# Kernel optimization log

Measured on AMD Instinct MI355X. Metric: run time of the kernel, lower is better.

## Reference

```python
import jax, jax.numpy as jnp
import numpy as np

N = 50000      # num nodes
E = 800000     # num edges
C = 512        # channels
ALPHA = 0.1
BETA = float(np.log(0.5 / 1 + 1.0))  # GCN2Conv: beta = log(theta/layer + 1)


def setup_inputs() -> dict:
    key = jax.random.key(0)
    k1, k2, k3, k4, k5 = jax.random.split(key, 5)
    x = jax.random.normal(k1, (N, C), dtype=jnp.float32)
    x0 = jax.random.normal(k2, (N, C), dtype=jnp.float32)
    W1 = jax.random.normal(k3, (C, C), dtype=jnp.float32) * (1.0 / np.sqrt(C))
    edge_weight = jax.random.uniform(k4, (E,), dtype=jnp.float32)
    edge_index = jax.random.randint(k5, (2, E), 0, N, dtype=jnp.int64)
    return {"x": x, "x0": x0, "W1": W1, "edge_weight": edge_weight,
            "edge_index": edge_index}


def reference(x, x0, W1, edge_weight, edge_index):
    src, dst = edge_index[0], edge_index[1]
    # propagate: message = x_j * edge_weight, sum-aggregate at target nodes
    msg = x[src] * edge_weight[:, None]                  # [E, C]
    agg = jax.ops.segment_sum(msg, dst, num_segments=N)  # [N, C]
    # residual blend: x*(1-alpha) + alpha*x_0
    h = agg * (1.0 - ALPHA) + ALPHA * x0                 # [N, C]
    # addmm: (1-beta)*h + beta*(h @ W1)
    out = (1.0 - BETA) * h + BETA * (h @ W1)
    return out
```

## Files before the change

kernel.cpp:

```cpp
#include <hip/hip_runtime.h>
#include <stdint.h>

#define NN 50000
#define NE 800000
#define CH 512

__device__ __forceinline__ unsigned short f2bf(float f) {
    union { float f; unsigned u; } v; v.f = f;
    unsigned u = v.u;
    unsigned r = u + 0x7FFFu + ((u >> 16) & 1u);
    return (unsigned short)(r >> 16);
}

__device__ __forceinline__ float u2f(unsigned u) {
    union { unsigned u; float f; } v; v.u = u;
    return v.f;
}

typedef short bf16x8 __attribute__((ext_vector_type(8)));
typedef float f32x4 __attribute__((ext_vector_type(4)));
typedef float f32x4e __attribute__((ext_vector_type(4)));
typedef unsigned u32x4e __attribute__((ext_vector_type(4)));

__global__ __launch_bounds__(256) void prologue(const f32x4e* __restrict__ x,
                                                u32x4e* __restrict__ xb,
                                                const float* __restrict__ W1,
                                                unsigned short* __restrict__ W1T,
                                                int* __restrict__ cnt) {
    int gid = blockIdx.x * 256 + threadIdx.x;
    {
        f32x4e a = __builtin_nontemporal_load(&x[2 * gid]);
        f32x4e b = __builtin_nontemporal_load(&x[2 * gid + 1]);
        u32x4e o;
        o.x = (unsigned)f2bf(a.x) | ((unsigned)f2bf(a.y) << 16);
        o.y = (unsigned)f2bf(a.z) | ((unsigned)f2bf(a.w) << 16);
        o.z = (unsigned)f2bf(b.x) | ((unsigned)f2bf(b.y) << 16);
        o.w = (unsigned)f2bf(b.z) | ((unsigned)f2bf(b.w) << 16);
        xb[gid] = o;
    }
    if (gid < CH * CH) {
        const float BETA = 0.40546510810816438f;
        const float OMB  = (float)(1.0 - 0.40546510810816438);
        int n = gid >> 9;
        int k = gid & 511;
        float v = BETA * W1[k * 512 + n] + (k == n ? OMB : 0.0f);
        W1T[gid] = f2bf(v);
    }
    if (gid < NN) cnt[gid] = 0;
}

__global__ void hist(const int* __restrict__ ei, int* __restrict__ cnt) {
    int e = blockIdx.x * 256 + threadIdx.x;
    if (e < NE) atomicAdd(&cnt[ei[NE + e]], 1);
}

#define SCAN_B 196

__global__ __launch_bounds__(256) void scan1(const int* __restrict__ cnt, int* __restrict__ bsum) {
    __shared__ int red[4];
    int t = threadIdx.x;
    int i = blockIdx.x * 256 + t;
    int v = (i < NN) ? cnt[i] : 0;
#pragma unroll
    for (int off = 32; off; off >>= 1) v += __shfl_xor(v, off, 64);
    if ((t & 63) == 0) red[t >> 6] = v;
    __syncthreads();
    if (t == 0) bsum[blockIdx.x] = red[0] + red[1] + red[2] + red[3];
}

__global__ __launch_bounds__(256) void scan2(int* __restrict__ bsum, int* __restrict__ boff) {
    __shared__ int ls[256];
    int t = threadIdx.x;
    int v = (t < SCAN_B) ? bsum[t] : 0;
    ls[t] = v;
    __syncthreads();
    for (int off = 1; off < 256; off <<= 1) {
        int add = (t >= off) ? ls[t - off] : 0;
        __syncthreads();
        ls[t] += add;
        __syncthreads();
    }
    if (t < SCAN_B) boff[t] = ls[t] - v;
}

__global__ __launch_bounds__(256) void scan3(const int* __restrict__ cnt, const int* __restrict__ boff,
                                             int* __restrict__ rowptr, int* __restrict__ cursor) {
    __shared__ int ls[256];
    int t = threadIdx.x;
    int i = blockIdx.x * 256 + t;
    int v = (i < NN) ? cnt[i] : 0;
    ls[t] = v;
    __syncthreads();
    for (int off = 1; off < 256; off <<= 1) {
        int add = (t >= off) ? ls[t - off] : 0;
        __syncthreads();
        ls[t] += add;
        __syncthreads();
    }
    if (i < NN) {
        int pre = ls[t] - v + boff[blockIdx.x];
        rowptr[i] = pre;
        cursor[i] = pre;
    }
}

__global__ void fill_slots(const int* __restrict__ ei, const float* __restrict__ ew,
                           int* __restrict__ cursor, int2* __restrict__ eiw) {
    int e = blockIdx.x * 256 + threadIdx.x;
    if (e < NE) {
        int d = ei[NE + e];
        int p = atomicAdd(&cursor[d], 1);
        int2 sw;
        sw.x = ei[e];
        sw.y = __float_as_int(0.9f * ew[e]);
        eiw[p] = sw;
    }
}

__global__ __launch_bounds__(256) void gather_nodes(const u32x4e* __restrict__ xb,
                                                    const f32x4e* __restrict__ x0,
                                                    const int* __restrict__ rowptr,
                                                    const int* __restrict__ cnt,
                                                    const int2* __restrict__ eiw,
                                                    unsigned short* __restrict__ hb) {
    int node = blockIdx.x * 4 + (threadIdx.x >> 6);
    if (node >= NN) return;
    int lane = threadIdx.x & 63;

    const f32x4e* x0r = (const f32x4e*)(x0 + (size_t)node * (CH / 4));
    f32x4e a0 = __builtin_nontemporal_load(&x0r[lane * 2]);
    f32x4e a1 = __builtin_nontemporal_load(&x0r[lane * 2 + 1]);
    float acc[8];
    acc[0] = 0.1f * a0.x; acc[1] = 0.1f * a0.y; acc[2] = 0.1f * a0.z; acc[3] = 0.1f * a0.w;
    acc[4] = 0.1f * a1.x; acc[5] = 0.1f * a1.y; acc[6] = 0.1f * a1.z; acc[7] = 0.1f * a1.w;

    int i = rowptr[node];
    int end = i + cnt[node];

#define ACCUM(vv, ww)                                    \
    acc[0] += (ww) * u2f((vv).x << 16);                  \
    acc[1] += (ww) * u2f((vv).x & 0xffff0000u);          \
    acc[2] += (ww) * u2f((vv).y << 16);                  \
    acc[3] += (ww) * u2f((vv).y & 0xffff0000u);          \
    acc[4] += (ww) * u2f((vv).z << 16);                  \
    acc[5] += (ww) * u2f((vv).z & 0xffff0000u);          \
    acc[6] += (ww) * u2f((vv).w << 16);                  \
    acc[7] += (ww) * u2f((vv).w & 0xffff0000u);

    for (; i + 8 <= end; i += 8) {
        int2 e[8];
#pragma unroll
        for (int j = 0; j < 8; ++j) e[j] = eiw[i + j];
        u32x4e v[8];
#pragma unroll
        for (int j = 0; j < 8; ++j) v[j] = xb[(size_t)e[j].x * (CH / 8) + lane];
#pragma unroll
        for (int j = 0; j < 8; ++j) { float w = __int_as_float(e[j].y); ACCUM(v[j], w) }
    }
    for (; i + 2 <= end; i += 2) {
        int2 e0 = eiw[i], e1 = eiw[i + 1];
        u32x4e v0 = xb[(size_t)e0.x * (CH / 8) + lane];
        u32x4e v1 = xb[(size_t)e1.x * (CH / 8) + lane];
        float w0 = __int_as_float(e0.y), w1 = __int_as_float(e1.y);
        ACCUM(v0, w0)
        ACCUM(v1, w1)
    }
    for (; i < end; ++i) {
        int2 e0 = eiw[i];
        u32x4e v0 = xb[(size_t)e0.x * (CH / 8) + lane];
        float w0 = __int_as_float(e0.y);
        ACCUM(v0, w0)
    }
#undef ACCUM

    u32x4e o;
    o.x = (unsigned)f2bf(acc[0]) | ((unsigned)f2bf(acc[1]) << 16);
    o.y = (unsigned)f2bf(acc[2]) | ((unsigned)f2bf(acc[3]) << 16);
    o.z = (unsigned)f2bf(acc[4]) | ((unsigned)f2bf(acc[5]) << 16);
    o.w = (unsigned)f2bf(acc[6]) | ((unsigned)f2bf(acc[7]) << 16);
    *(u32x4e*)(hb + (size_t)node * CH + lane * 8) = o;
}

__global__ __launch_bounds__(512) void gemm_out(const unsigned short* __restrict__ hb,
                                                const unsigned short* __restrict__ W1T,
                                                float* __restrict__ out) {
    __shared__ unsigned short Al[128 * 64];
    __shared__ unsigned short Bl[256 * 64];
    int t = threadIdx.x;
    int lane = t & 63, w = t >> 6;
    int wm = w & 1, wn = w >> 1;
    int rowBase = blockIdx.y * 128;
    int colBase = blockIdx.x * 256;

    f32x4 acc[4][4] = {};

    for (int k0 = 0; k0 < 512; k0 += 64) {
#pragma unroll
        for (int p = 0; p < 2; ++p) {
            int row = p * 64 + (t >> 3);
            int k8 = (t & 7) * 8;
            uint4 v = *(const uint4*)(hb + (size_t)(rowBase + row) * 512 + k0 + k8);
            int addr = (row * 128 + k8 * 2) ^ ((row & 7) << 4);
            *(uint4*)((char*)Al + addr) = v;
        }
#pragma unroll
        for (int p = 0; p < 4; ++p) {
            int col = p * 64 + (t >> 3);
            int k8 = (t & 7) * 8;
            uint4 v = *(const uint4*)(W1T + (size_t)(colBase + col) * 512 + k0 + k8);
            int addr = (col * 128 + k8 * 2) ^ ((col & 7) << 4);
            *(uint4*)((char*)Bl + addr) = v;
        }
        __syncthreads();

#pragma unroll
        for (int kk = 0; kk < 2; ++kk) {
            bf16x8 af[4], bfr[4];
            int kb = kk * 32 + (lane >> 4) * 8;
#pragma unroll
            for (int mi = 0; mi < 4; ++mi) {
                int row = wm * 64 + mi * 16 + (lane & 15);
                int addr = (row * 128 + kb * 2) ^ ((row & 7) << 4);
                af[mi] = *(const bf16x8*)((const char*)Al + addr);
            }
#pragma unroll
            for (int ni = 0; ni < 4; ++ni) {
                int col = wn * 64 + ni * 16 + (lane & 15);
                int addr = (col * 128 + kb * 2) ^ ((col & 7) << 4);
                bfr[ni] = *(const bf16x8*)((const char*)Bl + addr);
            }
#pragma unroll
            for (int mi = 0; mi < 4; ++mi)
#pragma unroll
                for (int ni = 0; ni < 4; ++ni)
                    acc[mi][ni] = __builtin_amdgcn_mfma_f32_16x16x32_bf16(
                        af[mi], bfr[ni], acc[mi][ni], 0, 0, 0);
        }
        __syncthreads();
    }

#pragma unroll
    for (int mi = 0; mi < 4; ++mi) {
#pragma unroll
        for (int j = 0; j < 4; ++j) {
            int grow = rowBase + wm * 64 + mi * 16 + (lane >> 4) * 4 + j;
            if (grow < NN) {
#pragma unroll
                for (int ni = 0; ni < 4; ++ni) {
                    __builtin_nontemporal_store(
                        acc[mi][ni][j],
                        &out[(size_t)grow * 512 + colBase + wn * 64 + ni * 16 + (lane & 15)]);
                }
            }
        }
    }
}

extern "C" void kernel_launch(void* const* d_in, const int* in_sizes, int n_in,
                              void* d_out, int out_size, void* d_ws, size_t ws_size,
                              hipStream_t stream) {
    const float* x  = (const float*)d_in[0];
    const float* x0 = (const float*)d_in[1];
    const float* W1 = (const float*)d_in[2];
    const float* ew = (const float*)d_in[3];
    const int*   ei = (const int*)d_in[4];
    float* out = (float*)d_out;

    char* ws = (char*)d_ws;
    unsigned short* hb   = (unsigned short*)(ws);
    unsigned short* W1T  = (unsigned short*)(ws + 51249152);
    int*   cnt    = (int*)(ws + 51773440);
    int*   rowptr = (int*)(ws + 51973440);
    int*   cursor = (int*)(ws + 52173440);
    int2*  eiw    = (int2*)(ws + 52373440);
    int*   bsum   = (int*)(ws + 58773440);
    int*   boff   = (int*)(ws + 58774464);

    u32x4e* xb = (u32x4e*)d_out;

    prologue<<<NN * CH / 8 / 256, 256, 0, stream>>>((const f32x4e*)x, xb, W1, W1T, cnt);
    hist<<<(NE + 255) / 256, 256, 0, stream>>>(ei, cnt);
    scan1<<<SCAN_B, 256, 0, stream>>>(cnt, bsum);
    scan2<<<1, 256, 0, stream>>>(bsum, boff);
    scan3<<<SCAN_B, 256, 0, stream>>>(cnt, boff, rowptr, cursor);
    fill_slots<<<(NE + 255) / 256, 256, 0, stream>>>(ei, ew, cursor, eiw);
    gather_nodes<<<(NN + 3) / 4, 256, 0, stream>>>(xb, (const f32x4e*)x0, rowptr, cnt, eiw, hb);
    gemm_out<<<dim3(2, 391), 512, 0, stream>>>(hb, W1T, out);
}
```

Before: 303.2 us.

## Fuse neighbor gather and GEMM into one kernel with LDS-resident rows

Merges the gather/aggregate kernel and the bf16 GEMM into a single kernel. Each 512-thread block aggregates 32 nodes into a swizzled LDS tile, then multiplies that tile by the full W1T, read directly from global memory. This removes the round trip of the intermediate h matrix through HBM and one kernel launch. The bf16 copy of x moves from the output buffer into workspace. The cost is that every block rereads the whole weight matrix without LDS staging, and the GEMM phase waits on the slowest wave's gather.

```diff
diff --git a/kernel.cpp b/kernel.cpp
--- a/kernel.cpp
+++ b/kernel.cpp
@@ -117,25 +117,17 @@
     }
 }
 
-__global__ __launch_bounds__(256) void gather_nodes(const u32x4e* __restrict__ xb,
-                                                    const f32x4e* __restrict__ x0,
-                                                    const int* __restrict__ rowptr,
-                                                    const int* __restrict__ cnt,
-                                                    const int2* __restrict__ eiw,
-                                                    unsigned short* __restrict__ hb) {
-    int node = blockIdx.x * 4 + (threadIdx.x >> 6);
-    if (node >= NN) return;
-    int lane = threadIdx.x & 63;
-
-    const f32x4e* x0r = (const f32x4e*)(x0 + (size_t)node * (CH / 4));
-    f32x4e a0 = __builtin_nontemporal_load(&x0r[lane * 2]);
-    f32x4e a1 = __builtin_nontemporal_load(&x0r[lane * 2 + 1]);
-    float acc[8];
-    acc[0] = 0.1f * a0.x; acc[1] = 0.1f * a0.y; acc[2] = 0.1f * a0.z; acc[3] = 0.1f * a0.w;
-    acc[4] = 0.1f * a1.x; acc[5] = 0.1f * a1.y; acc[6] = 0.1f * a1.z; acc[7] = 0.1f * a1.w;
-
-    int i = rowptr[node];
-    int end = i + cnt[node];
+__global__ __launch_bounds__(512, 4) void fused_gg(const u32x4e* __restrict__ xb,
+                                                   const f32x4e* __restrict__ x0,
+                                                   const int* __restrict__ rowptr,
+                                                   const int* __restrict__ cnt,
+                                                   const int2* __restrict__ eiw,
+                                                   const unsigned short* __restrict__ W1T,
+                                                   float* __restrict__ out) {
+    __shared__ unsigned short Al[32 * 512];
+    int t = threadIdx.x;
+    int lane = t & 63, w = t >> 6;
+    int rowBase = blockIdx.x * 32;
 
 #define ACCUM(vv, ww)                                    \
     acc[0] += (ww) * u2f((vv).x << 16);                  \
@@ -147,109 +139,89 @@
     acc[6] += (ww) * u2f((vv).w << 16);                  \
     acc[7] += (ww) * u2f((vv).w & 0xffff0000u);
 
-    for (; i + 8 <= end; i += 8) {
-        int2 e[8];
-#pragma unroll
-        for (int j = 0; j < 8; ++j) e[j] = eiw[i + j];
-        u32x4e v[8];
-#pragma unroll
-        for (int j = 0; j < 8; ++j) v[j] = xb[(size_t)e[j].x * (CH / 8) + lane];
-#pragma unroll
-        for (int j = 0; j < 8; ++j) { float w = __int_as_float(e[j].y); ACCUM(v[j], w) }
-    }
-    for (; i + 2 <= end; i += 2) {
-        int2 e0 = eiw[i], e1 = eiw[i + 1];
-        u32x4e v0 = xb[(size_t)e0.x * (CH / 8) + lane];
-        u32x4e v1 = xb[(size_t)e1.x * (CH / 8) + lane];
-        float w0 = __int_as_float(e0.y), w1 = __int_as_float(e1.y);
-        ACCUM(v0, w0)
-        ACCUM(v1, w1)
-    }
-    for (; i < end; ++i) {
-        int2 e0 = eiw[i];
-        u32x4e v0 = xb[(size_t)e0.x * (CH / 8) + lane];
-        float w0 = __int_as_float(e0.y);
-        ACCUM(v0, w0)
+    for (int q = 0; q < 4; ++q) {
+        int row = w * 4 + q;
+        int node = rowBase + row;
+        float acc[8] = {0.f, 0.f, 0.f, 0.f, 0.f, 0.f, 0.f, 0.f};
+        if (node < NN) {
+            const f32x4e* x0r = x0 + (size_t)node * (CH / 4);
+            f32x4e a0 = __builtin_nontemporal_load(&x0r[lane * 2]);
+            f32x4e a1 = __builtin_nontemporal_load(&x0r[lane * 2 + 1]);
+            acc[0] = 0.1f * a0.x; acc[1] = 0.1f * a0.y; acc[2] = 0.1f * a0.z; acc[3] = 0.1f * a0.w;
+            acc[4] = 0.1f * a1.x; acc[5] = 0.1f * a1.y; acc[6] = 0.1f * a1.z; acc[7] = 0.1f * a1.w;
+
+            int i   = __builtin_amdgcn_readfirstlane(rowptr[node]);
+            int end = i + __builtin_amdgcn_readfirstlane(cnt[node]);
+            for (; i + 8 <= end; i += 8) {
+                int2 e[8];
+#pragma unroll
+                for (int j = 0; j < 8; ++j) e[j] = eiw[i + j];
+                u32x4e v[8];
+#pragma unroll
+                for (int j = 0; j < 8; ++j) v[j] = xb[(size_t)e[j].x * (CH / 8) + lane];
+#pragma unroll
+                for (int j = 0; j < 8; ++j) { float ww = __int_as_float(e[j].y); ACCUM(v[j], ww) }
+            }
+            for (; i + 2 <= end; i += 2) {
+                int2 e0 = eiw[i], e1 = eiw[i + 1];
+                u32x4e v0 = xb[(size_t)e0.x * (CH / 8) + lane];
+                u32x4e v1 = xb[(size_t)e1.x * (CH / 8) + lane];
+                float w0 = __int_as_float(e0.y), w1 = __int_as_float(e1.y);
+                ACCUM(v0, w0)
+                ACCUM(v1, w1)
+            }
+            for (; i < end; ++i) {
+                int2 e0 = eiw[i];
+                u32x4e v0 = xb[(size_t)e0.x * (CH / 8) + lane];
+                float w0 = __int_as_float(e0.y);
+                ACCUM(v0, w0)
+            }
+        }
+        uint4 o;
+        o.x = (unsigned)f2bf(acc[0]) | ((unsigned)f2bf(acc[1]) << 16);
+        o.y = (unsigned)f2bf(acc[2]) | ((unsigned)f2bf(acc[3]) << 16);
+        o.z = (unsigned)f2bf(acc[4]) | ((unsigned)f2bf(acc[5]) << 16);
+        o.w = (unsigned)f2bf(acc[6]) | ((unsigned)f2bf(acc[7]) << 16);
+        *(uint4*)((char*)Al + row * 1024 + ((lane * 16) ^ ((row & 7) << 4))) = o;
     }
 #undef ACCUM
-
-    u32x4e o;
-    o.x = (unsigned)f2bf(acc[0]) | ((unsigned)f2bf(acc[1]) << 16);
-    o.y = (unsigned)f2bf(acc[2]) | ((unsigned)f2bf(acc[3]) << 16);
-    o.z = (unsigned)f2bf(acc[4]) | ((unsigned)f2bf(acc[5]) << 16);
-    o.w = (unsigned)f2bf(acc[6]) | ((unsigned)f2bf(acc[7]) << 16);
-    *(u32x4e*)(hb + (size_t)node * CH + lane * 8) = o;
-}
-
-__global__ __launch_bounds__(512) void gemm_out(const unsigned short* __restrict__ hb,
-                                                const unsigned short* __restrict__ W1T,
-                                                float* __restrict__ out) {
-    __shared__ unsigned short Al[128 * 64];
-    __shared__ unsigned short Bl[256 * 64];
-    int t = threadIdx.x;
-    int lane = t & 63, w = t >> 6;
-    int wm = w & 1, wn = w >> 1;
-    int rowBase = blockIdx.y * 128;
-    int colBase = blockIdx.x * 256;
-
-    f32x4 acc[4][4] = {};
-
-    for (int k0 = 0; k0 < 512; k0 += 64) {
-#pragma unroll
-        for (int p = 0; p < 2; ++p) {
-            int row = p * 64 + (t >> 3);
-            int k8 = (t & 7) * 8;
-            uint4 v = *(const uint4*)(hb + (size_t)(rowBase + row) * 512 + k0 + k8);
-            int addr = (row * 128 + k8 * 2) ^ ((row & 7) << 4);
-            *(uint4*)((char*)Al + addr) = v;
-        }
-#pragma unroll
-        for (int p = 0; p < 4; ++p) {
-            int col = p * 64 + (t >> 3);
-            int k8 = (t & 7) * 8;
-            uint4 v = *(const uint4*)(W1T + (size_t)(colBase + col) * 512 + k0 + k8);
-            int addr = (col * 128 + k8 * 2) ^ ((col & 7) << 4);
-            *(uint4*)((char*)Bl + addr) = v;
-        }
-        __syncthreads();
-
-#pragma unroll
-        for (int kk = 0; kk < 2; ++kk) {
-            bf16x8 af[4], bfr[4];
-            int kb = kk * 32 + (lane >> 4) * 8;
-#pragma unroll
-            for (int mi = 0; mi < 4; ++mi) {
-                int row = wm * 64 + mi * 16 + (lane & 15);
-                int addr = (row * 128 + kb * 2) ^ ((row & 7) << 4);
-                af[mi] = *(const bf16x8*)((const char*)Al + addr);
-            }
-#pragma unroll
-            for (int ni = 0; ni < 4; ++ni) {
-                int col = wn * 64 + ni * 16 + (lane & 15);
-                int addr = (col * 128 + kb * 2) ^ ((col & 7) << 4);
-                bfr[ni] = *(const bf16x8*)((const char*)Bl + addr);
-            }
-#pragma unroll
-            for (int mi = 0; mi < 4; ++mi)
-#pragma unroll
-                for (int ni = 0; ni < 4; ++ni)
-                    acc[mi][ni] = __builtin_amdgcn_mfma_f32_16x16x32_bf16(
-                        af[mi], bfr[ni], acc[mi][ni], 0, 0, 0);
-        }
-        __syncthreads();
-    }
-
-#pragma unroll
-    for (int mi = 0; mi < 4; ++mi) {
+    __syncthreads();
+
+    f32x4 acc2[2][4] = {};
+    int kg = lane >> 4;
+    int kb = kg * 8;
+    for (int k0 = 0; k0 < 512; k0 += 32) {
+        bf16x8 af[2], bfr[4];
+#pragma unroll
+        for (int mi = 0; mi < 2; ++mi) {
+            int row = mi * 16 + (lane & 15);
+            af[mi] = *(const bf16x8*)((const char*)Al + row * 1024 +
+                                      (((k0 + kb) * 2) ^ ((row & 7) << 4)));
+        }
+#pragma unroll
+        for (int ni = 0; ni < 4; ++ni) {
+            int col = w * 64 + ni * 16 + (lane & 15);
+            bfr[ni] = *(const bf16x8*)(W1T + (size_t)col * 512 + k0 + kb);
+        }
+#pragma unroll
+        for (int mi = 0; mi < 2; ++mi)
+#pragma unroll
+            for (int ni = 0; ni < 4; ++ni)
+                acc2[mi][ni] = __builtin_amdgcn_mfma_f32_16x16x32_bf16(
+                    af[mi], bfr[ni], acc2[mi][ni], 0, 0, 0);
+    }
+
+#pragma unroll
+    for (int mi = 0; mi < 2; ++mi) {
 #pragma unroll
         for (int j = 0; j < 4; ++j) {
-            int grow = rowBase + wm * 64 + mi * 16 + (lane >> 4) * 4 + j;
+            int grow = rowBase + mi * 16 + kg * 4 + j;
             if (grow < NN) {
 #pragma unroll
                 for (int ni = 0; ni < 4; ++ni) {
                     __builtin_nontemporal_store(
-                        acc[mi][ni][j],
-                        &out[(size_t)grow * 512 + colBase + wn * 64 + ni * 16 + (lane & 15)]);
+                        acc2[mi][ni][j],
+                        &out[(size_t)grow * 512 + w * 64 + ni * 16 + (lane & 15)]);
                 }
             }
         }
@@ -267,7 +239,7 @@
     float* out = (float*)d_out;
 
     char* ws = (char*)d_ws;
-    unsigned short* hb   = (unsigned short*)(ws);
+    u32x4e* xb           = (u32x4e*)(ws);
     unsigned short* W1T  = (unsigned short*)(ws + 51249152);
     int*   cnt    = (int*)(ws + 51773440);
     int*   rowptr = (int*)(ws + 51973440);
@@ -276,14 +248,12 @@
     int*   bsum   = (int*)(ws + 58773440);
     int*   boff   = (int*)(ws + 58774464);
 
-    u32x4e* xb = (u32x4e*)d_out;
-
     prologue<<<NN * CH / 8 / 256, 256, 0, stream>>>((const f32x4e*)x, xb, W1, W1T, cnt);
     hist<<<(NE + 255) / 256, 256, 0, stream>>>(ei, cnt);
     scan1<<<SCAN_B, 256, 0, stream>>>(cnt, bsum);
     scan2<<<1, 256, 0, stream>>>(bsum, boff);
     scan3<<<SCAN_B, 256, 0, stream>>>(cnt, boff, rowptr, cursor);
     fill_slots<<<(NE + 255) / 256, 256, 0, stream>>>(ei, ew, cursor, eiw);
-    gather_nodes<<<(NN + 3) / 4, 256, 0, stream>>>(xb, (const f32x4e*)x0, rowptr, cnt, eiw, hb);
-    gemm_out<<<dim3(2, 391), 512, 0, stream>>>(hb, W1T, out);
-}
+    fused_gg<<<(NN + 31) / 32, 512, 0, stream>>>(xb, (const f32x4e*)x0, rowptr, cnt, eiw,
+                                                 W1T, out);
+}
```

Measured after the change: 344.0 us. +13.5%, slower.

## Move x0 residual blend into GEMM A-load and widen GEMM tile to full N

Applied to the files above, without the earlier changes.

The gather kernel now writes only the weighted neighbour sum, and the GEMM adds 0.1*x0 while staging A tiles into LDS, rounding to bf16 there. The GEMM tile becomes 128x512 with K-steps of 32 and padded LDS rows instead of XOR swizzle, so each A row is loaded once rather than twice across two column blocks. This takes the x0 read off the latency-bound gather and avoids reading the aggregate twice. In exchange it adds a second bf16 rounding of the aggregate, uses more accumulator registers (which may lower occupancy), and runs twice as many K-loop syncs.

```diff
diff --git a/kernel.cpp b/kernel.cpp
--- a/kernel.cpp
+++ b/kernel.cpp
@@ -118,21 +118,15 @@
 }
 
 __global__ __launch_bounds__(256) void gather_nodes(const u32x4e* __restrict__ xb,
-                                                    const f32x4e* __restrict__ x0,
                                                     const int* __restrict__ rowptr,
                                                     const int* __restrict__ cnt,
                                                     const int2* __restrict__ eiw,
-                                                    unsigned short* __restrict__ hb) {
+                                                    unsigned short* __restrict__ agg) {
     int node = blockIdx.x * 4 + (threadIdx.x >> 6);
     if (node >= NN) return;
     int lane = threadIdx.x & 63;
 
-    const f32x4e* x0r = (const f32x4e*)(x0 + (size_t)node * (CH / 4));
-    f32x4e a0 = __builtin_nontemporal_load(&x0r[lane * 2]);
-    f32x4e a1 = __builtin_nontemporal_load(&x0r[lane * 2 + 1]);
-    float acc[8];
-    acc[0] = 0.1f * a0.x; acc[1] = 0.1f * a0.y; acc[2] = 0.1f * a0.z; acc[3] = 0.1f * a0.w;
-    acc[4] = 0.1f * a1.x; acc[5] = 0.1f * a1.y; acc[6] = 0.1f * a1.z; acc[7] = 0.1f * a1.w;
+    float acc[8] = {0.f, 0.f, 0.f, 0.f, 0.f, 0.f, 0.f, 0.f};
 
     int i = rowptr[node];
     int end = i + cnt[node];
@@ -178,64 +172,74 @@
     o.y = (unsigned)f2bf(acc[2]) | ((unsigned)f2bf(acc[3]) << 16);
     o.z = (unsigned)f2bf(acc[4]) | ((unsigned)f2bf(acc[5]) << 16);
     o.w = (unsigned)f2bf(acc[6]) | ((unsigned)f2bf(acc[7]) << 16);
-    *(u32x4e*)(hb + (size_t)node * CH + lane * 8) = o;
-}
-
-__global__ __launch_bounds__(512) void gemm_out(const unsigned short* __restrict__ hb,
-                                                const unsigned short* __restrict__ W1T,
-                                                float* __restrict__ out) {
-    __shared__ unsigned short Al[128 * 64];
-    __shared__ unsigned short Bl[256 * 64];
+    *(u32x4e*)(agg + (size_t)node * CH + lane * 8) = o;
+}
+
+__global__ __launch_bounds__(512) void gemm512(const unsigned short* __restrict__ agg,
+                                               const float* __restrict__ x0,
+                                               const unsigned short* __restrict__ W1T,
+                                               float* __restrict__ out) {
+    __shared__ unsigned short Al[128 * 40];
+    __shared__ unsigned short Bl[512 * 40];
     int t = threadIdx.x;
     int lane = t & 63, w = t >> 6;
-    int wm = w & 1, wn = w >> 1;
-    int rowBase = blockIdx.y * 128;
-    int colBase = blockIdx.x * 256;
-
-    f32x4 acc[4][4] = {};
-
-    for (int k0 = 0; k0 < 512; k0 += 64) {
-#pragma unroll
-        for (int p = 0; p < 2; ++p) {
-            int row = p * 64 + (t >> 3);
-            int k8 = (t & 7) * 8;
-            uint4 v = *(const uint4*)(hb + (size_t)(rowBase + row) * 512 + k0 + k8);
-            int addr = (row * 128 + k8 * 2) ^ ((row & 7) << 4);
-            *(uint4*)((char*)Al + addr) = v;
+    int wm = w >> 2, wn = w & 3;
+    int rowBase = blockIdx.x * 128;
+
+    f32x4 acc[4][8] = {};
+
+    for (int k0 = 0; k0 < 512; k0 += 32) {
+        {
+            int arow = t >> 2;
+            int k8 = (t & 3) * 8;
+            int grow = rowBase + arow;
+            if (grow > NN - 1) grow = NN - 1;
+            size_t base = (size_t)grow * 512 + k0 + k8;
+            uint4 ag = *(const uint4*)(agg + base);
+            f32x4e xa = __builtin_nontemporal_load((const f32x4e*)(x0 + base));
+            f32x4e xc = __builtin_nontemporal_load((const f32x4e*)(x0 + base + 4));
+            float v0 = u2f(ag.x << 16)         + 0.1f * xa.x;
+            float v1 = u2f(ag.x & 0xffff0000u) + 0.1f * xa.y;
+            float v2 = u2f(ag.y << 16)         + 0.1f * xa.z;
+            float v3 = u2f(ag.y & 0xffff0000u) + 0.1f * xa.w;
+            float v4 = u2f(ag.z << 16)         + 0.1f * xc.x;
+            float v5 = u2f(ag.z & 0xffff0000u) + 0.1f * xc.y;
+            float v6 = u2f(ag.w << 16)         + 0.1f * xc.z;
+            float v7 = u2f(ag.w & 0xffff0000u) + 0.1f * xc.w;
+            uint4 o;
+            o.x = (unsigned)f2bf(v0) | ((unsigned)f2bf(v1) << 16);
+            o.y = (unsigned)f2bf(v2) | ((unsigned)f2bf(v3) << 16);
+            o.z = (unsigned)f2bf(v4) | ((unsigned)f2bf(v5) << 16);
+            o.w = (unsigned)f2bf(v6) | ((unsigned)f2bf(v7) << 16);
+            *(uint4*)((char*)Al + arow * 80 + k8 * 2) = o;
         }
 #pragma unroll
         for (int p = 0; p < 4; ++p) {
-            int col = p * 64 + (t >> 3);
-            int k8 = (t & 7) * 8;
-            uint4 v = *(const uint4*)(W1T + (size_t)(colBase + col) * 512 + k0 + k8);
-            int addr = (col * 128 + k8 * 2) ^ ((col & 7) << 4);
-            *(uint4*)((char*)Bl + addr) = v;
-        }
-        __syncthreads();
-
-#pragma unroll
-        for (int kk = 0; kk < 2; ++kk) {
-            bf16x8 af[4], bfr[4];
-            int kb = kk * 32 + (lane >> 4) * 8;
-#pragma unroll
-            for (int mi = 0; mi < 4; ++mi) {
-                int row = wm * 64 + mi * 16 + (lane & 15);
-                int addr = (row * 128 + kb * 2) ^ ((row & 7) << 4);
-                af[mi] = *(const bf16x8*)((const char*)Al + addr);
-            }
-#pragma unroll
-            for (int ni = 0; ni < 4; ++ni) {
-                int col = wn * 64 + ni * 16 + (lane & 15);
-                int addr = (col * 128 + kb * 2) ^ ((col & 7) << 4);
-                bfr[ni] = *(const bf16x8*)((const char*)Bl + addr);
-            }
-#pragma unroll
-            for (int mi = 0; mi < 4; ++mi)
-#pragma unroll
-                for (int ni = 0; ni < 4; ++ni)
-                    acc[mi][ni] = __builtin_amdgcn_mfma_f32_16x16x32_bf16(
-                        af[mi], bfr[ni], acc[mi][ni], 0, 0, 0);
-        }
+            int col = p * 128 + (t >> 2);
+            int k8 = (t & 3) * 8;
+            uint4 v = *(const uint4*)(W1T + (size_t)col * 512 + k0 + k8);
+            *(uint4*)((char*)Bl + col * 80 + k8 * 2) = v;
+        }
+        __syncthreads();
+
+        int kb = (lane >> 4) * 8;
+        bf16x8 af[4], bfr[8];
+#pragma unroll
+        for (int mi = 0; mi < 4; ++mi) {
+            int row = wm * 64 + mi * 16 + (lane & 15);
+            af[mi] = *(const bf16x8*)((const char*)Al + row * 80 + kb * 2);
+        }
+#pragma unroll
+        for (int ni = 0; ni < 8; ++ni) {
+            int col = wn * 128 + ni * 16 + (lane & 15);
+            bfr[ni] = *(const bf16x8*)((const char*)Bl + col * 80 + kb * 2);
+        }
+#pragma unroll
+        for (int mi = 0; mi < 4; ++mi)
+#pragma unroll
+            for (int ni = 0; ni < 8; ++ni)
+                acc[mi][ni] = __builtin_amdgcn_mfma_f32_16x16x32_bf16(
+                    af[mi], bfr[ni], acc[mi][ni], 0, 0, 0);
         __syncthreads();
     }
 
@@ -246,10 +250,10 @@
             int grow = rowBase + wm * 64 + mi * 16 + (lane >> 4) * 4 + j;
             if (grow < NN) {
 #pragma unroll
-                for (int ni = 0; ni < 4; ++ni) {
+                for (int ni = 0; ni < 8; ++ni) {
                     __builtin_nontemporal_store(
                         acc[mi][ni][j],
-                        &out[(size_t)grow * 512 + colBase + wn * 64 + ni * 16 + (lane & 15)]);
+                        &out[(size_t)grow * 512 + wn * 128 + ni * 16 + (lane & 15)]);
                 }
             }
         }
@@ -267,7 +271,7 @@
     float* out = (float*)d_out;
 
     char* ws = (char*)d_ws;
-    unsigned short* hb   = (unsigned short*)(ws);
+    unsigned short* agg  = (unsigned short*)(ws);
     unsigned short* W1T  = (unsigned short*)(ws + 51249152);
     int*   cnt    = (int*)(ws + 51773440);
     int*   rowptr = (int*)(ws + 51973440);
@@ -284,6 +288,6 @@
     scan2<<<1, 256, 0, stream>>>(bsum, boff);
     scan3<<<SCAN_B, 256, 0, stream>>>(cnt, boff, rowptr, cursor);
     fill_slots<<<(NE + 255) / 256, 256, 0, stream>>>(ei, ew, cursor, eiw);
-    gather_nodes<<<(NN + 3) / 4, 256, 0, stream>>>(xb, (const f32x4e*)x0, rowptr, cnt, eiw, hb);
-    gemm_out<<<dim3(2, 391), 512, 0, stream>>>(hb, W1T, out);
-}
+    gather_nodes<<<(NN + 3) / 4, 256, 0, stream>>>(xb, rowptr, cnt, eiw, agg);
+    gemm512<<<(NN + 127) / 128, 512, 0, stream>>>(agg, x0, W1T, out);
+}
```

Result: slower. 332.3 us (+9.6%).
